# Kernel tuning notes

Measured on AMD Instinct MI355X. Metric: run time of the kernel, lower is better.

The kernel has to match this reference:

```python
import jax, jax.numpy as jnp
import numpy as np
from jax import lax

H = 32  # input_size == hidden_size
NUM_CLASSES = 10


def setup_inputs() -> dict:
    key = jax.random.key(0)
    ks = jax.random.split(key, 12)
    s = 1.0 / np.sqrt(H)  # torch default uniform(-1/sqrt(H), 1/sqrt(H))
    u = lambda k, shape: jax.random.uniform(k, shape, jnp.float32, -s, s)
    return {
        "x": jax.random.normal(ks[0], (512, 2048, H), jnp.float32),
        "W_ih0": u(ks[1], (H, H)),
        "W_hh0": u(ks[2], (H, H)),
        "b_ih0": u(ks[3], (H,)),
        "b_hh0": u(ks[4], (H,)),
        "W_ih1": u(ks[5], (H, H)),
        "W_hh1": u(ks[6], (H, H)),
        "b_ih1": u(ks[7], (H,)),
        "b_hh1": u(ks[8], (H,)),
        "fc_w": u(ks[9], (NUM_CLASSES, H)),
        "fc_b": u(ks[10], (NUM_CLASSES,)),
    }


def reference(x, W_ih0, W_hh0, b_ih0, b_hh0, W_ih1, W_hh1, b_ih1, b_hh1, fc_w, fc_b):
    # x: [B, T, H]; 2-layer tanh RNN, return logits from final hidden of layer 2.
    B = x.shape[0]
    h0 = jnp.zeros((B, H), x.dtype)

    def step(carry, x_t):
        h1, h2 = carry
        h1 = jnp.tanh(x_t @ W_ih0.T + b_ih0 + h1 @ W_hh0.T + b_hh0)
        h2 = jnp.tanh(h1 @ W_ih1.T + b_ih1 + h2 @ W_hh1.T + b_hh1)
        return (h1, h2), None

    xT = jnp.swapaxes(x, 0, 1)  # [T, B, H] for scan over time
    (_, h2_final), _ = lax.scan(step, (h0, h0), xT)
    return h2_final @ fc_w.T + fc_b  # [B, NUM_CLASSES]
```

## Files before the change

### kernel.cpp

```cpp
#include <hip/hip_runtime.h>

#define RH 32
#define RT 2048
#define RB 512
#define RC 10

#define XRING 0
#define H1OFF 512
#define H2OFF 544
#define TRASH 576
#define LDSF  608

__device__ __forceinline__ float fast_tanh(float x) {
    float e = __builtin_amdgcn_exp2f(x * 2.88539008177792681472f);
    return fmaf(-2.0f, __builtin_amdgcn_rcpf(e + 1.0f), 1.0f);
}

__global__ __launch_bounds__(64) void rnn2_kernel(
    const float* __restrict__ x,
    const float* __restrict__ W_ih0, const float* __restrict__ W_hh0,
    const float* __restrict__ b_ih0, const float* __restrict__ b_hh0,
    const float* __restrict__ W_ih1, const float* __restrict__ W_hh1,
    const float* __restrict__ b_ih1, const float* __restrict__ b_hh1,
    const float* __restrict__ fc_w, const float* __restrict__ fc_b,
    float* __restrict__ out)
{
    __shared__ float lds[LDSF];
    const int b    = blockIdx.x;
    const int lane = threadIdx.x;
    const int j    = lane & 31;
    const int half = lane >> 5;

    const float* WA = half ? W_hh1 : W_hh0;
    const float* WB = half ? W_ih1 : W_ih0;
    float wa[RH], wb[RH];
#pragma unroll
    for (int q = 0; q < 8; ++q) {
        float4 va = *(const float4*)&WA[j * RH + q * 4];
        float4 vb = *(const float4*)&WB[j * RH + q * 4];
        wa[q*4+0]=va.x; wa[q*4+1]=va.y; wa[q*4+2]=va.z; wa[q*4+3]=va.w;
        wb[q*4+0]=vb.x; wb[q*4+1]=vb.y; wb[q*4+2]=vb.z; wb[q*4+3]=vb.w;
    }
    const float bias = half ? (b_ih1[j] + b_hh1[j]) : (b_ih0[j] + b_hh0[j]);

    if (lane < RH) { lds[H1OFF + lane] = 0.0f; lds[H2OFF + lane] = 0.0f; }
    __syncthreads();

    const float* pA  = &lds[half ? H2OFF : H1OFF];
    const float* ph1 = &lds[H1OFF];
    float* wr_norm   = &lds[(half ? H2OFF : H1OFF) + j];
    float* wr_first  = half ? &lds[TRASH + j] : &lds[H1OFF + j];
    float* wr_last   = half ? &lds[H2OFF + j] : &lds[TRASH + j];

    const float* xg = x + (size_t)b * RT * RH + lane * 4;
#define STAGE(c)  __builtin_amdgcn_global_load_lds( \
        (const __attribute__((address_space(1))) void*)(xg + (c) * 256), \
        (__attribute__((address_space(3))) void*)&lds[XRING + ((c) & 1) * 256], \
        16, 0, 0)

#define STEP(XB, S, WRP) do {                                                \
        const float4* Af = (const float4*)pA;                                \
        const float4* Bf = (const float4*)(half ? ph1 : ((XB) + (S) * RH));  \
        float sA0=0.f,sA1=0.f,sA2=0.f,sA3=0.f;                               \
        float sB0=0.f,sB1=0.f,sB2=0.f,sB3=0.f;                               \
        _Pragma("unroll")                                                    \
        for (int q = 0; q < 4; ++q) {                                        \
            float4 a0 = Af[q], a1 = Af[q+4];                                 \
            float4 b0 = Bf[q], b1 = Bf[q+4];                                 \
            sA0 = fmaf(wa[q*4+0], a0.x, sA0);                                \
            sA1 = fmaf(wa[q*4+1], a0.y, sA1);                                \
            sA2 = fmaf(wa[q*4+2], a0.z, sA2);                                \
            sA3 = fmaf(wa[q*4+3], a0.w, sA3);                                \
            sA0 = fmaf(wa[16+q*4+0], a1.x, sA0);                             \
            sA1 = fmaf(wa[16+q*4+1], a1.y, sA1);                             \
            sA2 = fmaf(wa[16+q*4+2], a1.z, sA2);                             \
            sA3 = fmaf(wa[16+q*4+3], a1.w, sA3);                             \
            sB0 = fmaf(wb[q*4+0], b0.x, sB0);                                \
            sB1 = fmaf(wb[q*4+1], b0.y, sB1);                                \
            sB2 = fmaf(wb[q*4+2], b0.z, sB2);                                \
            sB3 = fmaf(wb[q*4+3], b0.w, sB3);                                \
            sB0 = fmaf(wb[16+q*4+0], b1.x, sB0);                             \
            sB1 = fmaf(wb[16+q*4+1], b1.y, sB1);                             \
            sB2 = fmaf(wb[16+q*4+2], b1.z, sB2);                             \
            sB3 = fmaf(wb[16+q*4+3], b1.w, sB3);                             \
        }                                                                    \
        float r = ((sA0+sA1)+(sA2+sA3)) + ((sB0+sB1)+(sB2+sB3));             \
        *(WRP) = fast_tanh(r + bias);                                        \
        __asm__ volatile("" ::: "memory");                                   \
    } while (0)

    STAGE(0);
    STAGE(1);

    STAGE(2);
    __asm__ volatile("s_waitcnt vmcnt(2)" ::: "memory");
    {
        const float* xb = &lds[XRING];
        STEP(xb, 0, wr_first);
        STEP(xb, 1, wr_norm); STEP(xb, 2, wr_norm); STEP(xb, 3, wr_norm);
        STEP(xb, 4, wr_norm); STEP(xb, 5, wr_norm); STEP(xb, 6, wr_norm);
        STEP(xb, 7, wr_norm);
    }
    for (int c = 1; c <= 253; ++c) {
        STAGE(c + 2);
        __asm__ volatile("s_waitcnt vmcnt(2)" ::: "memory");
        const float* xb = &lds[XRING + (c & 1) * 256];
        STEP(xb, 0, wr_norm); STEP(xb, 1, wr_norm); STEP(xb, 2, wr_norm);
        STEP(xb, 3, wr_norm); STEP(xb, 4, wr_norm); STEP(xb, 5, wr_norm);
        STEP(xb, 6, wr_norm); STEP(xb, 7, wr_norm);
    }
    __asm__ volatile("s_waitcnt vmcnt(1)" ::: "memory");
    {
        const float* xb = &lds[XRING];
        STEP(xb, 0, wr_norm); STEP(xb, 1, wr_norm); STEP(xb, 2, wr_norm);
        STEP(xb, 3, wr_norm); STEP(xb, 4, wr_norm); STEP(xb, 5, wr_norm);
        STEP(xb, 6, wr_norm); STEP(xb, 7, wr_norm);
    }
    __asm__ volatile("s_waitcnt vmcnt(0)" ::: "memory");
    {
        const float* xb = &lds[XRING + 256];
        STEP(xb, 0, wr_norm); STEP(xb, 1, wr_norm); STEP(xb, 2, wr_norm);
        STEP(xb, 3, wr_norm); STEP(xb, 4, wr_norm); STEP(xb, 5, wr_norm);
        STEP(xb, 6, wr_norm); STEP(xb, 7, wr_norm);
    }
    {
        const float* xb = &lds[XRING];
        STEP(xb, 0, wr_last);
    }
#undef STEP
#undef STAGE

    if (lane < RC) {
        float s = fc_b[lane];
#pragma unroll
        for (int k = 0; k < RH; ++k)
            s = fmaf(fc_w[lane * RH + k], lds[H2OFF + k], s);
        out[b * RC + lane] = s;
    }
}

extern "C" void kernel_launch(void* const* d_in, const int* in_sizes, int n_in,
                              void* d_out, int out_size, void* d_ws, size_t ws_size,
                              hipStream_t stream) {
    const float* x     = (const float*)d_in[0];
    const float* W_ih0 = (const float*)d_in[1];
    const float* W_hh0 = (const float*)d_in[2];
    const float* b_ih0 = (const float*)d_in[3];
    const float* b_hh0 = (const float*)d_in[4];
    const float* W_ih1 = (const float*)d_in[5];
    const float* W_hh1 = (const float*)d_in[6];
    const float* b_ih1 = (const float*)d_in[7];
    const float* b_hh1 = (const float*)d_in[8];
    const float* fc_w  = (const float*)d_in[9];
    const float* fc_b  = (const float*)d_in[10];
    float* out = (float*)d_out;

    rnn2_kernel<<<RB, 64, 0, stream>>>(x, W_ih0, W_hh0, b_ih0, b_hh0,
                                       W_ih1, W_hh1, b_ih1, b_hh1,
                                       fc_w, fc_b, out);
}
```

Baseline: 484.8 us.

## Process two batch rows per wave with each half-wave running both layers

Each 64-lane block now handles two sequences: each 32-lane half computes both RNN layers for its own batch row, with layer 2 lagging layer 1 by one step (wavefront pipelining across layers). The launch is halved to 256 blocks and the x staging ring grows to four slots per sequence. The aim is to raise per-lane work and cut the grid so the serial per-step chain is shared across two rows. The cost is four 32-float weight arrays held in registers per lane, which raises register pressure, and twice the FMAs per step per lane.

```diff
diff --git a/kernel.cpp b/kernel.cpp
--- a/kernel.cpp
+++ b/kernel.cpp
@@ -2,14 +2,14 @@
 
 #define RH 32
 #define RT 2048
-#define RB 512
 #define RC 10
 
-#define XRING 0
-#define H1OFF 512
-#define H2OFF 544
-#define TRASH 576
-#define LDSF  608
+#define XR0   0
+#define XR1   1024
+#define H1O   2048
+#define H2O   2112
+#define TRO   2176
+#define LDSF  2208
 
 __device__ __forceinline__ float fast_tanh(float x) {
     float e = __builtin_amdgcn_exp2f(x * 2.88539008177792681472f);
@@ -26,116 +26,124 @@
     float* __restrict__ out)
 {
     __shared__ float lds[LDSF];
-    const int b    = blockIdx.x;
+    const int blk  = blockIdx.x;
     const int lane = threadIdx.x;
+    const int g    = lane >> 5;
     const int j    = lane & 31;
-    const int half = lane >> 5;
 
-    const float* WA = half ? W_hh1 : W_hh0;
-    const float* WB = half ? W_ih1 : W_ih0;
-    float wa[RH], wb[RH];
+    const float* xA = x + (size_t)(2 * blk) * RT * RH;
+    const float* xB = xA + (size_t)RT * RH;
+
+    float w0[RH], wh0[RH], w1[RH], wh1[RH];
 #pragma unroll
     for (int q = 0; q < 8; ++q) {
-        float4 va = *(const float4*)&WA[j * RH + q * 4];
-        float4 vb = *(const float4*)&WB[j * RH + q * 4];
-        wa[q*4+0]=va.x; wa[q*4+1]=va.y; wa[q*4+2]=va.z; wa[q*4+3]=va.w;
-        wb[q*4+0]=vb.x; wb[q*4+1]=vb.y; wb[q*4+2]=vb.z; wb[q*4+3]=vb.w;
+        float4 a = *(const float4*)&W_ih0[j * RH + q * 4];
+        float4 b = *(const float4*)&W_hh0[j * RH + q * 4];
+        float4 c = *(const float4*)&W_ih1[j * RH + q * 4];
+        float4 d = *(const float4*)&W_hh1[j * RH + q * 4];
+        w0 [q*4+0]=a.x; w0 [q*4+1]=a.y; w0 [q*4+2]=a.z; w0 [q*4+3]=a.w;
+        wh0[q*4+0]=b.x; wh0[q*4+1]=b.y; wh0[q*4+2]=b.z; wh0[q*4+3]=b.w;
+        w1 [q*4+0]=c.x; w1 [q*4+1]=c.y; w1 [q*4+2]=c.z; w1 [q*4+3]=c.w;
+        wh1[q*4+0]=d.x; wh1[q*4+1]=d.y; wh1[q*4+2]=d.z; wh1[q*4+3]=d.w;
     }
-    const float bias = half ? (b_ih1[j] + b_hh1[j]) : (b_ih0[j] + b_hh0[j]);
+    const float bias1 = b_ih0[j] + b_hh0[j];
+    const float bias2 = b_ih1[j] + b_hh1[j];
 
-    if (lane < RH) { lds[H1OFF + lane] = 0.0f; lds[H2OFF + lane] = 0.0f; }
+    lds[H1O + lane] = 0.0f;
+    lds[H2O + lane] = 0.0f;
     __syncthreads();
 
-    const float* pA  = &lds[half ? H2OFF : H1OFF];
-    const float* ph1 = &lds[H1OFF];
-    float* wr_norm   = &lds[(half ? H2OFF : H1OFF) + j];
-    float* wr_first  = half ? &lds[TRASH + j] : &lds[H1OFF + j];
-    float* wr_last   = half ? &lds[H2OFF + j] : &lds[TRASH + j];
+    const int xbase = g * 1024;
+    float* const h1w = &lds[H1O + g * 32 + j];
+    float* const h2w = &lds[H2O + g * 32 + j];
+    float* const trw = &lds[TRO + j];
 
-    const float* xg = x + (size_t)b * RT * RH + lane * 4;
-#define STAGE(c)  __builtin_amdgcn_global_load_lds( \
-        (const __attribute__((address_space(1))) void*)(xg + (c) * 256), \
-        (__attribute__((address_space(3))) void*)&lds[XRING + ((c) & 1) * 256], \
-        16, 0, 0)
+#define STAGE2(c) do {                                                        \
+    __builtin_amdgcn_global_load_lds(                                         \
+        (const __attribute__((address_space(1))) void*)(xA + (c) * 256 + lane * 4), \
+        (__attribute__((address_space(3))) void*)&lds[XR0 + ((c) & 3) * 256], \
+        16, 0, 0);                                                            \
+    __builtin_amdgcn_global_load_lds(                                         \
+        (const __attribute__((address_space(1))) void*)(xB + (c) * 256 + lane * 4), \
+        (__attribute__((address_space(3))) void*)&lds[XR1 + ((c) & 3) * 256], \
+        16, 0, 0);                                                            \
+} while (0)
 
-#define STEP(XB, S, WRP) do {                                                \
-        const float4* Af = (const float4*)pA;                                \
-        const float4* Bf = (const float4*)(half ? ph1 : ((XB) + (S) * RH));  \
-        float sA0=0.f,sA1=0.f,sA2=0.f,sA3=0.f;                               \
-        float sB0=0.f,sB1=0.f,sB2=0.f,sB3=0.f;                               \
-        _Pragma("unroll")                                                    \
-        for (int q = 0; q < 4; ++q) {                                        \
-            float4 a0 = Af[q], a1 = Af[q+4];                                 \
-            float4 b0 = Bf[q], b1 = Bf[q+4];                                 \
-            sA0 = fmaf(wa[q*4+0], a0.x, sA0);                                \
-            sA1 = fmaf(wa[q*4+1], a0.y, sA1);                                \
-            sA2 = fmaf(wa[q*4+2], a0.z, sA2);                                \
-            sA3 = fmaf(wa[q*4+3], a0.w, sA3);                                \
-            sA0 = fmaf(wa[16+q*4+0], a1.x, sA0);                             \
-            sA1 = fmaf(wa[16+q*4+1], a1.y, sA1);                             \
-            sA2 = fmaf(wa[16+q*4+2], a1.z, sA2);                             \
-            sA3 = fmaf(wa[16+q*4+3], a1.w, sA3);                             \
-            sB0 = fmaf(wb[q*4+0], b0.x, sB0);                                \
-            sB1 = fmaf(wb[q*4+1], b0.y, sB1);                                \
-            sB2 = fmaf(wb[q*4+2], b0.z, sB2);                                \
-            sB3 = fmaf(wb[q*4+3], b0.w, sB3);                                \
-            sB0 = fmaf(wb[16+q*4+0], b1.x, sB0);                             \
-            sB1 = fmaf(wb[16+q*4+1], b1.y, sB1);                             \
-            sB2 = fmaf(wb[16+q*4+2], b1.z, sB2);                             \
-            sB3 = fmaf(wb[16+q*4+3], b1.w, sB3);                             \
-        }                                                                    \
-        float r = ((sA0+sA1)+(sA2+sA3)) + ((sB0+sB1)+(sB2+sB3));             \
-        *(WRP) = fast_tanh(r + bias);                                        \
-        __asm__ volatile("" ::: "memory");                                   \
-    } while (0)
+#define STEP(SB, S, H1D, H2D) do {                                           \
+    const float4* xp = (const float4*)&lds[(SB) + (S) * 32];                 \
+    const float4* ap = (const float4*)&lds[H1O + g * 32];                    \
+    const float4* bp = (const float4*)&lds[H2O + g * 32];                    \
+    float ax0=0.f, ax1=0.f, ah0=0.f, ah1=0.f;                                \
+    float ba0=0.f, ba1=0.f, bb0=0.f, bb1=0.f;                                \
+    _Pragma("unroll")                                                        \
+    for (int q = 0; q < 8; ++q) {                                            \
+        float4 xv = xp[q]; float4 av = ap[q]; float4 bv = bp[q];             \
+        ax0 = fmaf(w0 [q*4+0], xv.x, ax0);                                   \
+        ax1 = fmaf(w0 [q*4+1], xv.y, ax1);                                   \
+        ah0 = fmaf(wh0[q*4+0], av.x, ah0);                                   \
+        ah1 = fmaf(wh0[q*4+1], av.y, ah1);                                   \
+        ba0 = fmaf(w1 [q*4+0], av.x, ba0);                                   \
+        ba1 = fmaf(w1 [q*4+1], av.y, ba1);                                   \
+        bb0 = fmaf(wh1[q*4+0], bv.x, bb0);                                   \
+        bb1 = fmaf(wh1[q*4+1], bv.y, bb1);                                   \
+        ax0 = fmaf(w0 [q*4+2], xv.z, ax0);                                   \
+        ax1 = fmaf(w0 [q*4+3], xv.w, ax1);                                   \
+        ah0 = fmaf(wh0[q*4+2], av.z, ah0);                                   \
+        ah1 = fmaf(wh0[q*4+3], av.w, ah1);                                   \
+        ba0 = fmaf(w1 [q*4+2], av.z, ba0);                                   \
+        ba1 = fmaf(w1 [q*4+3], av.w, ba1);                                   \
+        bb0 = fmaf(wh1[q*4+2], bv.z, bb0);                                   \
+        bb1 = fmaf(wh1[q*4+3], bv.w, bb1);                                   \
+    }                                                                        \
+    float a1 = (ax0 + ax1) + (ah0 + ah1) + bias1;                            \
+    float a2 = (ba0 + ba1) + (bb0 + bb1) + bias2;                            \
+    *(H1D) = fast_tanh(a1);                                                  \
+    *(H2D) = fast_tanh(a2);                                                  \
+    __asm__ volatile("" ::: "memory");                                       \
+} while (0)
 
-    STAGE(0);
-    STAGE(1);
+    STAGE2(0); STAGE2(1); STAGE2(2);
+    __asm__ volatile("s_waitcnt vmcnt(4)" ::: "memory");
 
-    STAGE(2);
-    __asm__ volatile("s_waitcnt vmcnt(2)" ::: "memory");
     {
-        const float* xb = &lds[XRING];
-        STEP(xb, 0, wr_first);
-        STEP(xb, 1, wr_norm); STEP(xb, 2, wr_norm); STEP(xb, 3, wr_norm);
-        STEP(xb, 4, wr_norm); STEP(xb, 5, wr_norm); STEP(xb, 6, wr_norm);
-        STEP(xb, 7, wr_norm);
+        const int sb = xbase;
+        STEP(sb, 0, h1w, trw);
+        STEP(sb, 1, h1w, h2w); STEP(sb, 2, h1w, h2w); STEP(sb, 3, h1w, h2w);
+        STEP(sb, 4, h1w, h2w); STEP(sb, 5, h1w, h2w); STEP(sb, 6, h1w, h2w);
+        STEP(sb, 7, h1w, h2w);
     }
     for (int c = 1; c <= 253; ++c) {
-        STAGE(c + 2);
-        __asm__ volatile("s_waitcnt vmcnt(2)" ::: "memory");
-        const float* xb = &lds[XRING + (c & 1) * 256];
-        STEP(xb, 0, wr_norm); STEP(xb, 1, wr_norm); STEP(xb, 2, wr_norm);
-        STEP(xb, 3, wr_norm); STEP(xb, 4, wr_norm); STEP(xb, 5, wr_norm);
-        STEP(xb, 6, wr_norm); STEP(xb, 7, wr_norm);
-    }
-    __asm__ volatile("s_waitcnt vmcnt(1)" ::: "memory");
-    {
-        const float* xb = &lds[XRING];
-        STEP(xb, 0, wr_norm); STEP(xb, 1, wr_norm); STEP(xb, 2, wr_norm);
-        STEP(xb, 3, wr_norm); STEP(xb, 4, wr_norm); STEP(xb, 5, wr_norm);
-        STEP(xb, 6, wr_norm); STEP(xb, 7, wr_norm);
-    }
-    __asm__ volatile("s_waitcnt vmcnt(0)" ::: "memory");
-    {
-        const float* xb = &lds[XRING + 256];
-        STEP(xb, 0, wr_norm); STEP(xb, 1, wr_norm); STEP(xb, 2, wr_norm);
-        STEP(xb, 3, wr_norm); STEP(xb, 4, wr_norm); STEP(xb, 5, wr_norm);
-        STEP(xb, 6, wr_norm); STEP(xb, 7, wr_norm);
+        STAGE2(c + 2);
+        __asm__ volatile("s_waitcnt vmcnt(4)" ::: "memory");
+        const int sb = xbase + (c & 3) * 256;
+        STEP(sb, 0, h1w, h2w); STEP(sb, 1, h1w, h2w); STEP(sb, 2, h1w, h2w);
+        STEP(sb, 3, h1w, h2w); STEP(sb, 4, h1w, h2w); STEP(sb, 5, h1w, h2w);
+        STEP(sb, 6, h1w, h2w); STEP(sb, 7, h1w, h2w);
     }
     {
-        const float* xb = &lds[XRING];
-        STEP(xb, 0, wr_last);
+        __asm__ volatile("s_waitcnt vmcnt(2)" ::: "memory");
+        const int sb = xbase + 2 * 256;
+        STEP(sb, 0, h1w, h2w); STEP(sb, 1, h1w, h2w); STEP(sb, 2, h1w, h2w);
+        STEP(sb, 3, h1w, h2w); STEP(sb, 4, h1w, h2w); STEP(sb, 5, h1w, h2w);
+        STEP(sb, 6, h1w, h2w); STEP(sb, 7, h1w, h2w);
     }
+    {
+        __asm__ volatile("s_waitcnt vmcnt(0)" ::: "memory");
+        const int sb = xbase + 3 * 256;
+        STEP(sb, 0, h1w, h2w); STEP(sb, 1, h1w, h2w); STEP(sb, 2, h1w, h2w);
+        STEP(sb, 3, h1w, h2w); STEP(sb, 4, h1w, h2w); STEP(sb, 5, h1w, h2w);
+        STEP(sb, 6, h1w, h2w); STEP(sb, 7, h1w, h2w);
+    }
+    STEP(xbase, 0, trw, h2w);
 #undef STEP
-#undef STAGE
+#undef STAGE2
 
-    if (lane < RC) {
-        float s = fc_b[lane];
+    if (j < RC) {
+        float s = fc_b[j];
 #pragma unroll
         for (int k = 0; k < RH; ++k)
-            s = fmaf(fc_w[lane * RH + k], lds[H2OFF + k], s);
-        out[b * RC + lane] = s;
+            s = fmaf(fc_w[j * RH + k], lds[H2O + g * 32 + k], s);
+        out[(size_t)(2 * blk + g) * RC + j] = s;
     }
 }
 
@@ -155,7 +163,7 @@
     const float* fc_b  = (const float*)d_in[10];
     float* out = (float*)d_out;
 
-    rnn2_kernel<<<RB, 64, 0, stream>>>(x, W_ih0, W_hh0, b_ih0, b_hh0,
-                                       W_ih1, W_hh1, b_ih1, b_hh1,
-                                       fc_w, fc_b, out);
+    rnn2_kernel<<<256, 64, 0, stream>>>(x, W_ih0, W_hh0, b_ih0, b_hh0,
+                                        W_ih1, W_hh1, b_ih1, b_hh1,
+                                        fc_w, fc_b, out);
 }
```

Result: slower. 917.5 us (+89.2%).

## Batch 16 sequences per wave and run recurrence on fp16 MFMA

Applied to the files above, without the earlier changes.

Replaces the one-sequence-per-workgroup FP32 dot-product RNN with a single wavefront handling 16 batch rows. Each time step runs as 16x16x32 fp16 MFMAs, and the hidden state stays in registers in the MFMA fragment layout, so there is no LDS round trip per step. x is prefetched four steps ahead straight into registers, and the grid drops from 512 workgroups to 32. This trades fp16 precision in the weights, inputs and hidden state across 2048 steps, and much lower GPU occupancy, for fewer instructions and less synchronisation on the serial critical path.

```diff
diff --git a/kernel.cpp b/kernel.cpp
--- a/kernel.cpp
+++ b/kernel.cpp
@@ -2,21 +2,30 @@
 
 #define RH 32
 #define RT 2048
-#define RB 512
 #define RC 10
 
-#define XRING 0
-#define H1OFF 512
-#define H2OFF 544
-#define TRASH 576
-#define LDSF  608
+typedef __attribute__((ext_vector_type(8))) _Float16 f16x8;
+typedef __attribute__((ext_vector_type(4))) float f32x4;
+
+#define MFMA16(a,b,c) __builtin_amdgcn_mfma_f32_16x16x32_f16((a),(b),(c),0,0,0)
 
 __device__ __forceinline__ float fast_tanh(float x) {
     float e = __builtin_amdgcn_exp2f(x * 2.88539008177792681472f);
     return fmaf(-2.0f, __builtin_amdgcn_rcpf(e + 1.0f), 1.0f);
 }
 
-__global__ __launch_bounds__(64) void rnn2_kernel(
+__device__ __forceinline__ f16x8 load_wfrag16(const float* __restrict__ W,
+                                              int base, int n, int g) {
+    f16x8 f;
+#pragma unroll
+    for (int e = 0; e < 8; ++e) {
+        int k = 4*g + (e & 3) + 16*(e >> 2);
+        f[e] = (_Float16)W[(base + n)*RH + k];
+    }
+    return f;
+}
+
+__global__ __launch_bounds__(64) void rnn2_mfma1w_kernel(
     const float* __restrict__ x,
     const float* __restrict__ W_ih0, const float* __restrict__ W_hh0,
     const float* __restrict__ b_ih0, const float* __restrict__ b_hh0,
@@ -25,117 +34,103 @@
     const float* __restrict__ fc_w, const float* __restrict__ fc_b,
     float* __restrict__ out)
 {
-    __shared__ float lds[LDSF];
-    const int b    = blockIdx.x;
-    const int lane = threadIdx.x;
-    const int j    = lane & 31;
-    const int half = lane >> 5;
+    __shared__ float h2fin[16][RH];
 
-    const float* WA = half ? W_hh1 : W_hh0;
-    const float* WB = half ? W_ih1 : W_ih0;
-    float wa[RH], wb[RH];
+    const int ln = threadIdx.x;
+    const int n  = ln & 15;
+    const int g  = ln >> 4;
+
+    f16x8 WI0a = load_wfrag16(W_ih0,  0, n, g);
+    f16x8 WI0b = load_wfrag16(W_ih0, 16, n, g);
+    f16x8 WH0a = load_wfrag16(W_hh0,  0, n, g);
+    f16x8 WH0b = load_wfrag16(W_hh0, 16, n, g);
+    f16x8 WI1a = load_wfrag16(W_ih1,  0, n, g);
+    f16x8 WI1b = load_wfrag16(W_ih1, 16, n, g);
+    f16x8 WH1a = load_wfrag16(W_hh1,  0, n, g);
+    f16x8 WH1b = load_wfrag16(W_hh1, 16, n, g);
+
+    f32x4 cb1a, cb1b, cb2a, cb2b;
 #pragma unroll
-    for (int q = 0; q < 8; ++q) {
-        float4 va = *(const float4*)&WA[j * RH + q * 4];
-        float4 vb = *(const float4*)&WB[j * RH + q * 4];
-        wa[q*4+0]=va.x; wa[q*4+1]=va.y; wa[q*4+2]=va.z; wa[q*4+3]=va.w;
-        wb[q*4+0]=vb.x; wb[q*4+1]=vb.y; wb[q*4+2]=vb.z; wb[q*4+3]=vb.w;
+    for (int i = 0; i < 4; ++i) {
+        cb1a[i] = b_ih0[4*g + i]      + b_hh0[4*g + i];
+        cb1b[i] = b_ih0[16 + 4*g + i] + b_hh0[16 + 4*g + i];
+        cb2a[i] = b_ih1[4*g + i]      + b_hh1[4*g + i];
+        cb2b[i] = b_ih1[16 + 4*g + i] + b_hh1[16 + 4*g + i];
     }
-    const float bias = half ? (b_ih1[j] + b_hh1[j]) : (b_ih0[j] + b_hh0[j]);
 
-    if (lane < RH) { lds[H1OFF + lane] = 0.0f; lds[H2OFF + lane] = 0.0f; }
+    f16x8 h1f, h2f;
+#pragma unroll
+    for (int e = 0; e < 8; ++e) { h1f[e] = (_Float16)0.0f; h2f[e] = (_Float16)0.0f; }
+
+    const float* xp = x + (size_t)(blockIdx.x*16 + n) * (RT*RH) + 4*g;
+    float4 A0, B0, A1, B1, A2, B2, A3, B3;
+
+#define PREF(A_, B_, T_) do { \
+    const float* p_ = xp + (size_t)(T_) * RH; \
+    A_ = *(const float4*)p_; \
+    B_ = *(const float4*)(p_ + 16); \
+} while (0)
+
+#define STEP(A_, B_, DOPREF, PT_) do { \
+    f16x8 xf_; \
+    { \
+        auto q0_ = __builtin_amdgcn_cvt_pkrtz(A_.x, A_.y); \
+        auto q1_ = __builtin_amdgcn_cvt_pkrtz(A_.z, A_.w); \
+        auto q2_ = __builtin_amdgcn_cvt_pkrtz(B_.x, B_.y); \
+        auto q3_ = __builtin_amdgcn_cvt_pkrtz(B_.z, B_.w); \
+        xf_[0] = q0_[0]; xf_[1] = q0_[1]; xf_[2] = q1_[0]; xf_[3] = q1_[1]; \
+        xf_[4] = q2_[0]; xf_[5] = q2_[1]; xf_[6] = q3_[0]; xf_[7] = q3_[1]; \
+    } \
+    if (DOPREF) { PREF(A_, B_, PT_); } \
+    f32x4 d0_ = MFMA16(WI0a, xf_, cb1a); \
+    f32x4 d1_ = MFMA16(WI0b, xf_, cb1b); \
+    d0_ = MFMA16(WH0a, h1f, d0_); \
+    d1_ = MFMA16(WH0b, h1f, d1_); \
+    _Pragma("unroll") \
+    for (int i_ = 0; i_ < 4; ++i_) { d0_[i_] = fast_tanh(d0_[i_]); d1_[i_] = fast_tanh(d1_[i_]); } \
+    _Pragma("unroll") \
+    for (int i_ = 0; i_ < 4; ++i_) { h1f[i_] = (_Float16)d0_[i_]; h1f[4+i_] = (_Float16)d1_[i_]; } \
+    f32x4 e0_ = MFMA16(WI1a, h1f, cb2a); \
+    f32x4 e1_ = MFMA16(WI1b, h1f, cb2b); \
+    e0_ = MFMA16(WH1a, h2f, e0_); \
+    e1_ = MFMA16(WH1b, h2f, e1_); \
+    _Pragma("unroll") \
+    for (int i_ = 0; i_ < 4; ++i_) { e0_[i_] = fast_tanh(e0_[i_]); e1_[i_] = fast_tanh(e1_[i_]); } \
+    _Pragma("unroll") \
+    for (int i_ = 0; i_ < 4; ++i_) { h2f[i_] = (_Float16)e0_[i_]; h2f[4+i_] = (_Float16)e1_[i_]; } \
+} while (0)
+
+    PREF(A0, B0, 0); PREF(A1, B1, 1); PREF(A2, B2, 2); PREF(A3, B3, 3);
+
+    for (int k = 0; k < 511; ++k) {
+        const int tb = 4*k;
+        STEP(A0, B0, 1, tb + 4);
+        STEP(A1, B1, 1, tb + 5);
+        STEP(A2, B2, 1, tb + 6);
+        STEP(A3, B3, 1, tb + 7);
+    }
+    STEP(A0, B0, 0, 0);
+    STEP(A1, B1, 0, 0);
+    STEP(A2, B2, 0, 0);
+    STEP(A3, B3, 0, 0);
+#undef STEP
+#undef PREF
+
+#pragma unroll
+    for (int i = 0; i < 4; ++i) {
+        h2fin[n][4*g + i]      = (float)h2f[i];
+        h2fin[n][16 + 4*g + i] = (float)h2f[4 + i];
+    }
     __syncthreads();
 
-    const float* pA  = &lds[half ? H2OFF : H1OFF];
-    const float* ph1 = &lds[H1OFF];
-    float* wr_norm   = &lds[(half ? H2OFF : H1OFF) + j];
-    float* wr_first  = half ? &lds[TRASH + j] : &lds[H1OFF + j];
-    float* wr_last   = half ? &lds[H2OFF + j] : &lds[TRASH + j];
-
-    const float* xg = x + (size_t)b * RT * RH + lane * 4;
-#define STAGE(c)  __builtin_amdgcn_global_load_lds( \
-        (const __attribute__((address_space(1))) void*)(xg + (c) * 256), \
-        (__attribute__((address_space(3))) void*)&lds[XRING + ((c) & 1) * 256], \
-        16, 0, 0)
-
-#define STEP(XB, S, WRP) do {                                                \
-        const float4* Af = (const float4*)pA;                                \
-        const float4* Bf = (const float4*)(half ? ph1 : ((XB) + (S) * RH));  \
-        float sA0=0.f,sA1=0.f,sA2=0.f,sA3=0.f;                               \
-        float sB0=0.f,sB1=0.f,sB2=0.f,sB3=0.f;                               \
-        _Pragma("unroll")                                                    \
-        for (int q = 0; q < 4; ++q) {                                        \
-            float4 a0 = Af[q], a1 = Af[q+4];                                 \
-            float4 b0 = Bf[q], b1 = Bf[q+4];                                 \
-            sA0 = fmaf(wa[q*4+0], a0.x, sA0);                                \
-            sA1 = fmaf(wa[q*4+1], a0.y, sA1);                                \
-            sA2 = fmaf(wa[q*4+2], a0.z, sA2);                                \
-            sA3 = fmaf(wa[q*4+3], a0.w, sA3);                                \
-            sA0 = fmaf(wa[16+q*4+0], a1.x, sA0);                             \
-            sA1 = fmaf(wa[16+q*4+1], a1.y, sA1);                             \
-            sA2 = fmaf(wa[16+q*4+2], a1.z, sA2);                             \
-            sA3 = fmaf(wa[16+q*4+3], a1.w, sA3);                             \
-            sB0 = fmaf(wb[q*4+0], b0.x, sB0);                                \
-            sB1 = fmaf(wb[q*4+1], b0.y, sB1);                                \
-            sB2 = fmaf(wb[q*4+2], b0.z, sB2);                                \
-            sB3 = fmaf(wb[q*4+3], b0.w, sB3);                                \
-            sB0 = fmaf(wb[16+q*4+0], b1.x, sB0);                             \
-            sB1 = fmaf(wb[16+q*4+1], b1.y, sB1);                             \
-            sB2 = fmaf(wb[16+q*4+2], b1.z, sB2);                             \
-            sB3 = fmaf(wb[16+q*4+3], b1.w, sB3);                             \
-        }                                                                    \
-        float r = ((sA0+sA1)+(sA2+sA3)) + ((sB0+sB1)+(sB2+sB3));             \
-        *(WRP) = fast_tanh(r + bias);                                        \
-        __asm__ volatile("" ::: "memory");                                   \
-    } while (0)
-
-    STAGE(0);
-    STAGE(1);
-
-    STAGE(2);
-    __asm__ volatile("s_waitcnt vmcnt(2)" ::: "memory");
-    {
-        const float* xb = &lds[XRING];
-        STEP(xb, 0, wr_first);
-        STEP(xb, 1, wr_norm); STEP(xb, 2, wr_norm); STEP(xb, 3, wr_norm);
-        STEP(xb, 4, wr_norm); STEP(xb, 5, wr_norm); STEP(xb, 6, wr_norm);
-        STEP(xb, 7, wr_norm);
-    }
-    for (int c = 1; c <= 253; ++c) {
-        STAGE(c + 2);
-        __asm__ volatile("s_waitcnt vmcnt(2)" ::: "memory");
-        const float* xb = &lds[XRING + (c & 1) * 256];
-        STEP(xb, 0, wr_norm); STEP(xb, 1, wr_norm); STEP(xb, 2, wr_norm);
-        STEP(xb, 3, wr_norm); STEP(xb, 4, wr_norm); STEP(xb, 5, wr_norm);
-        STEP(xb, 6, wr_norm); STEP(xb, 7, wr_norm);
-    }
-    __asm__ volatile("s_waitcnt vmcnt(1)" ::: "memory");
-    {
-        const float* xb = &lds[XRING];
-        STEP(xb, 0, wr_norm); STEP(xb, 1, wr_norm); STEP(xb, 2, wr_norm);
-        STEP(xb, 3, wr_norm); STEP(xb, 4, wr_norm); STEP(xb, 5, wr_norm);
-        STEP(xb, 6, wr_norm); STEP(xb, 7, wr_norm);
-    }
-    __asm__ volatile("s_waitcnt vmcnt(0)" ::: "memory");
-    {
-        const float* xb = &lds[XRING + 256];
-        STEP(xb, 0, wr_norm); STEP(xb, 1, wr_norm); STEP(xb, 2, wr_norm);
-        STEP(xb, 3, wr_norm); STEP(xb, 4, wr_norm); STEP(xb, 5, wr_norm);
-        STEP(xb, 6, wr_norm); STEP(xb, 7, wr_norm);
-    }
-    {
-        const float* xb = &lds[XRING];
-        STEP(xb, 0, wr_last);
-    }
-#undef STEP
-#undef STAGE
-
-    if (lane < RC) {
-        float s = fc_b[lane];
+    for (int c = ln; c < 16 * RC; c += 64) {
+        const int bt = c / RC;
+        const int cl = c % RC;
+        float s = fc_b[cl];
 #pragma unroll
-        for (int k = 0; k < RH; ++k)
-            s = fmaf(fc_w[lane * RH + k], lds[H2OFF + k], s);
-        out[b * RC + lane] = s;
+        for (int kk = 0; kk < RH; ++kk)
+            s = fmaf(fc_w[cl*RH + kk], h2fin[bt][kk], s);
+        out[(size_t)(blockIdx.x*16 + bt) * RC + cl] = s;
     }
 }
 
@@ -155,7 +150,7 @@
     const float* fc_b  = (const float*)d_in[10];
     float* out = (float*)d_out;
 
-    rnn2_kernel<<<RB, 64, 0, stream>>>(x, W_ih0, W_hh0, b_ih0, b_hh0,
-                                       W_ih1, W_hh1, b_ih1, b_hh1,
-                                       fc_w, fc_b, out);
+    rnn2_mfma1w_kernel<<<32, 64, 0, stream>>>(x, W_ih0, W_hh0, b_ih0, b_hh0,
+                                              W_ih1, W_hh1, b_ih1, b_hh1,
+                                              fc_w, fc_b, out);
 }
```

Result: slower. 622.3 us (+28.4%).
